# Kernel optimization log

Measured on AMD Instinct MI355X. Metric: run time of the kernel, lower is better.

The kernel has to match this reference:

```python
import jax, jax.numpy as jnp
import numpy as np

BATCH, LEN, DIM = 8, 4096, 512


def setup_inputs() -> dict:
    key = jax.random.key(0)
    k1, k2, k3, k4, k5 = jax.random.split(key, 5)
    x = jax.random.normal(k1, (BATCH, LEN, DIM), dtype=jnp.float32)
    hidden_real = jax.random.normal(k2, (BATCH, DIM), dtype=jnp.float32)
    hidden_imag = jax.random.normal(k3, (BATCH, DIM), dtype=jnp.float32)
    phazor_init = jax.random.normal(k4, (DIM, 2), dtype=jnp.float32)
    phazor_param = jax.random.normal(k5, (DIM, 2), dtype=jnp.float32)
    return {
        "x": x,
        "hidden_real": hidden_real,
        "hidden_imag": hidden_imag,
        "phazor_init": phazor_init,
        "phazor_param": phazor_param,
    }


def _forward(x, hidden, phazor_init, phazor_param):
    L = x.shape[1]
    # view_as_complex of the (dim, 2) real params
    pz = phazor_param[:, 0] + 1j * phazor_param[:, 1]           # [dim] complex
    pi = phazor_init[:, 0] + 1j * phazor_init[:, 1]             # [dim] complex
    # phazor = exp(-|z|^2) * exp(i * angle(z))
    phazor = jnp.exp(-(pz.real * pz.real + pz.imag * pz.imag)) * jnp.exp(1j * jnp.angle(pz))
    # phazor^t for t = 0..L-1  -> [L, dim]
    prog = jnp.power(phazor[None, :], jnp.arange(L, dtype=jnp.float32)[:, None])
    filt = prog * pi[None, :]                                   # [L, dim]
    filt_fft = jnp.fft.fft(filt, n=2 * L, axis=0)               # [2L, dim]
    x_fft = jnp.fft.fft(x.astype(jnp.complex64), n=2 * L, axis=1)  # [B, 2L, dim]
    conv = jnp.fft.ifft(filt_fft[None, :, :] * x_fft, axis=1)[:, :L, :]  # [B, L, dim]
    conv_with_past = conv + hidden[:, None, :] * prog[None, :, :] * phazor[None, None, :]
    return conv_with_past.real, conv_with_past


def reference(x, hidden_real, hidden_imag, phazor_init, phazor_param):
    hidden = hidden_real + 1j * hidden_imag
    out_real, out_complex = _forward(x, hidden, phazor_init, phazor_param)
    return out_real, out_complex
```

## Files before the change

### kernel.cpp

```cpp
#include <hip/hip_runtime.h>
#include <math.h>

#define B 8
#define L 4096
#define D 512
#define LC 64
#define CK (L / LC)
#define BLD ((size_t)B * L * D)

typedef float v2f __attribute__((ext_vector_type(2)));

#define WS_FLOATS (2 * B * CK * D)

__device__ __forceinline__ v2f phazor_of(const float* __restrict__ pparam, int d) {
    float a = pparam[d * 2 + 0];
    float bb = pparam[d * 2 + 1];
    float r2 = fmaf(a, a, bb * bb);
    float inv = rsqrtf(r2);
    inv = inv * fmaf(-0.5f * r2 * inv, inv, 1.5f);
    float mag = __expf(-r2);
    v2f p; p.x = mag * a * inv; p.y = mag * bb * inv;
    return p;
}

__global__ __launch_bounds__(256) void pass1_k(const float* __restrict__ x,
                                               const float* __restrict__ pparam,
                                               float* __restrict__ le) {
    int idx = blockIdx.x * blockDim.x + threadIdx.x;
    int d = idx % D;
    int c = (idx / D) % CK;
    int b = idx / (D * CK);
    v2f ph = phazor_of(pparam, d);
    float ur = 0.f, ui = 0.f;
    const float* xp = x + ((size_t)b * L + (size_t)c * LC) * D + d;
#pragma unroll 8
    for (int i = 0; i < LC; ++i) {
        float xv = xp[(size_t)i * D];
        float nr = fmaf(ph.x, ur, fmaf(-ph.y, ui, xv));
        float ni = fmaf(ph.x, ui, ph.y * ur);
        ur = nr;
        ui = ni;
    }
    v2f lv; lv.x = ur; lv.y = ui;
    *(v2f*)(le + (size_t)idx * 2) = lv;
}

template <int MODE>
__global__ __launch_bounds__(256) void pass2_k(const float* __restrict__ x,
                                               const float* __restrict__ hr,
                                               const float* __restrict__ hi,
                                               const float* __restrict__ pinit,
                                               const float* __restrict__ pparam,
                                               const float* __restrict__ le,
                                               float* __restrict__ out) {
    int idx = blockIdx.x * blockDim.x + threadIdx.x;
    int d = idx % D;
    int c = (idx / D) % CK;
    int b = idx / (D * CK);

    v2f ph = phazor_of(pparam, d);
    v2f q;  q.x = pinit[d * 2 + 0]; q.y = pinit[d * 2 + 1];

    float br = ph.x, bi = ph.y;
#pragma unroll
    for (int s = 0; s < 6; ++s) {
        float sr = fmaf(br, br, -bi * bi);
        float si = 2.f * br * bi;
        br = sr; bi = si;
    }

    float ur = 0.f, ui = 0.f;
    const float* lp = le + (((size_t)b * CK) * D + d) * 2;
    for (int j = 0; j < c; ++j) {
        v2f lv = *(const v2f*)(lp + (size_t)j * D * 2);
        float wr = fmaf(ur, br, fmaf(-ui, bi, lv.x));
        float wi = fmaf(ur, bi, fmaf(ui, br, lv.y));
        ur = wr; ui = wi;
    }

    float pwr = ph.x, pwi = ph.y;
    {
        float er = br, ei = bi;
        int n = c;
#pragma unroll
        for (int s = 0; s < 6; ++s) {
            if (n & 1) {
                float tr = fmaf(pwr, er, -pwi * ei);
                float ti = fmaf(pwr, ei, pwi * er);
                pwr = tr; pwi = ti;
            }
            float sr = fmaf(er, er, -ei * ei);
            float si = 2.f * er * ei;
            er = sr; ei = si;
            n >>= 1;
        }
    }

    float hre = hr[(size_t)b * D + d];
    float him = hi[(size_t)b * D + d];

    const float* xp = x + ((size_t)b * L + (size_t)c * LC) * D + d;
    float* outr = out + ((size_t)b * L + (size_t)c * LC) * D + d;
    float* outr2 = outr + BLD;
    float* outc = out + BLD + (((size_t)b * L + (size_t)c * LC) * D + d) * 2;

#pragma unroll 4
    for (int i = 0; i < LC; ++i) {
        float xv = xp[(size_t)i * D];
        float nr = fmaf(ph.x, ur, fmaf(-ph.y, ui, xv));
        float ni = fmaf(ph.x, ui, ph.y * ur);
        ur = nr;
        ui = ni;
        float vr = fmaf(q.x, ur, fmaf(-q.y, ui, fmaf(hre, pwr, -him * pwi)));
        float vi = fmaf(q.x, ui, fmaf(q.y, ur, fmaf(hre, pwi, him * pwr)));
        outr[(size_t)i * D] = vr;
        if (MODE == 0) {
            outr2[(size_t)i * D] = vr;
        } else {
            v2f vc; vc.x = vr; vc.y = vi;
            *(v2f*)(outc + (size_t)i * D * 2) = vc;
        }
        float tr = fmaf(pwr, ph.x, -pwi * ph.y);
        float ti = fmaf(pwr, ph.y, pwi * ph.x);
        pwr = tr;
        pwi = ti;
    }
}

template <int MODE>
__global__ __launch_bounds__(256) void fallback_k(const float* __restrict__ x,
                                                  const float* __restrict__ hr,
                                                  const float* __restrict__ hi,
                                                  const float* __restrict__ pinit,
                                                  const float* __restrict__ pparam,
                                                  float* __restrict__ out) {
    int idx = blockIdx.x * blockDim.x + threadIdx.x;
    if (idx >= B * D) return;
    int d = idx % D;
    int b = idx / D;
    v2f ph = phazor_of(pparam, d);
    float qr = pinit[d * 2 + 0];
    float qi = pinit[d * 2 + 1];
    float hre = hr[(size_t)b * D + d];
    float him = hi[(size_t)b * D + d];
    float ur = 0.f, ui = 0.f;
    float pwr = ph.x, pwi = ph.y;
    const float* xp = x + (size_t)b * L * D + d;
    float* outr = out + (size_t)b * L * D + d;
    float* outr2 = outr + BLD;
    float* outc = out + BLD + ((size_t)b * L * D + d) * 2;
    for (int t = 0; t < L; ++t) {
        float xv = xp[(size_t)t * D];
        float nr = fmaf(ph.x, ur, fmaf(-ph.y, ui, xv));
        float ni = fmaf(ph.x, ui, ph.y * ur);
        ur = nr; ui = ni;
        float vr = fmaf(qr, ur, fmaf(-qi, ui, fmaf(hre, pwr, -him * pwi)));
        float vi = fmaf(qr, ui, fmaf(qi, ur, fmaf(hre, pwi, him * pwr)));
        outr[(size_t)t * D] = vr;
        if (MODE == 0) {
            outr2[(size_t)t * D] = vr;
        } else {
            v2f vc; vc.x = vr; vc.y = vi;
            *(v2f*)(outc + (size_t)t * D * 2) = vc;
        }
        float tr = fmaf(pwr, ph.x, -pwi * ph.y);
        float ti = fmaf(pwr, ph.y, pwi * ph.x);
        pwr = tr; pwi = ti;
    }
}

extern "C" void kernel_launch(void* const* d_in, const int* in_sizes, int n_in,
                              void* d_out, int out_size, void* d_ws, size_t ws_size,
                              hipStream_t stream) {
    const float* x = (const float*)d_in[0];
    const float* hreal = (const float*)d_in[1];
    const float* himag = (const float*)d_in[2];
    const float* pinit = (const float*)d_in[3];
    const float* pparam = (const float*)d_in[4];
    float* le = (float*)d_ws;
    float* out = (float*)d_out;

    const int mode = (out_size >= (int)(3 * BLD)) ? 1 : 0;
    const bool fast = ws_size >= (size_t)WS_FLOATS * sizeof(float);

    if (fast) {
        int n = B * CK * D;
        pass1_k<<<n / 256, 256, 0, stream>>>(x, pparam, le);
        if (mode == 0)
            pass2_k<0><<<n / 256, 256, 0, stream>>>(x, hreal, himag, pinit, pparam, le, out);
        else
            pass2_k<1><<<n / 256, 256, 0, stream>>>(x, hreal, himag, pinit, pparam, le, out);
    } else {
        int n = B * D;
        if (mode == 0)
            fallback_k<0><<<(n + 255) / 256, 256, 0, stream>>>(x, hreal, himag, pinit, pparam, out);
        else
            fallback_k<1><<<(n + 255) / 256, 256, 0, stream>>>(x, hreal, himag, pinit, pparam, out);
    }
}
```

Baseline: 54.09 us.

## Add sequential carry kernel for chunk prefixes and halve chunk length

Adds a small carry kernel that turns per-chunk local end states into exclusive prefix carries with one sequential pass per (batch, dim). Each pass2 thread then reads its carry directly instead of re-scanning all earlier chunks, which was O(CK) work per thread. Chunk length drops from 64 to 32, doubling parallelism in pass1 and pass2, and the power-by-squaring loop in pass2 grows to 7 steps to cover the larger chunk index. The trade-off is an extra launch and a serial carry kernel of 128 steps with only 4096 threads.

```diff
diff --git a/kernel.cpp b/kernel.cpp
--- a/kernel.cpp
+++ b/kernel.cpp
@@ -4,13 +4,15 @@
 #define B 8
 #define L 4096
 #define D 512
-#define LC 64
+#define LC 32
 #define CK (L / LC)
 #define BLD ((size_t)B * L * D)
 
+#define NTH (B * CK * D)
+
+#define WS_FLOATS (2 * B * CK * D)
+
 typedef float v2f __attribute__((ext_vector_type(2)));
-
-#define WS_FLOATS (2 * B * CK * D)
 
 __device__ __forceinline__ v2f phazor_of(const float* __restrict__ pparam, int d) {
     float a = pparam[d * 2 + 0];
@@ -21,6 +23,18 @@
     float mag = __expf(-r2);
     v2f p; p.x = mag * a * inv; p.y = mag * bb * inv;
     return p;
+}
+
+__device__ __forceinline__ v2f p32_of(v2f ph) {
+    float br = ph.x, bi = ph.y;
+#pragma unroll
+    for (int s = 0; s < 5; ++s) {
+        float sr = fmaf(br, br, -bi * bi);
+        float si = 2.f * br * bi;
+        br = sr; bi = si;
+    }
+    v2f r; r.x = br; r.y = bi;
+    return r;
 }
 
 __global__ __launch_bounds__(256) void pass1_k(const float* __restrict__ x,
@@ -38,11 +52,29 @@
         float xv = xp[(size_t)i * D];
         float nr = fmaf(ph.x, ur, fmaf(-ph.y, ui, xv));
         float ni = fmaf(ph.x, ui, ph.y * ur);
-        ur = nr;
-        ui = ni;
+        ur = nr; ui = ni;
     }
     v2f lv; lv.x = ur; lv.y = ui;
     *(v2f*)(le + (size_t)idx * 2) = lv;
+}
+
+__global__ __launch_bounds__(256) void carry_k(const float* __restrict__ pparam,
+                                               float* __restrict__ le) {
+    int idx = blockIdx.x * blockDim.x + threadIdx.x;
+    int d = idx % D;
+    int b = idx / D;
+    v2f P = p32_of(phazor_of(pparam, d));
+    float wr = 0.f, wi = 0.f;
+    float* lp = le + (((size_t)b * CK) * D + d) * 2;
+#pragma unroll 4
+    for (int c = 0; c < CK; ++c) {
+        v2f lv = *(const v2f*)(lp + (size_t)c * D * 2);
+        v2f wv; wv.x = wr; wv.y = wi;
+        *(v2f*)(lp + (size_t)c * D * 2) = wv;
+        float tr = fmaf(P.x, wr, fmaf(-P.y, wi, lv.x));
+        float ti = fmaf(P.x, wi, fmaf(P.y, wr, lv.y));
+        wr = tr; wi = ti;
+    }
 }
 
 template <int MODE>
@@ -60,30 +92,17 @@
 
     v2f ph = phazor_of(pparam, d);
     v2f q;  q.x = pinit[d * 2 + 0]; q.y = pinit[d * 2 + 1];
-
-    float br = ph.x, bi = ph.y;
-#pragma unroll
-    for (int s = 0; s < 6; ++s) {
-        float sr = fmaf(br, br, -bi * bi);
-        float si = 2.f * br * bi;
-        br = sr; bi = si;
-    }
-
-    float ur = 0.f, ui = 0.f;
-    const float* lp = le + (((size_t)b * CK) * D + d) * 2;
-    for (int j = 0; j < c; ++j) {
-        v2f lv = *(const v2f*)(lp + (size_t)j * D * 2);
-        float wr = fmaf(ur, br, fmaf(-ui, bi, lv.x));
-        float wi = fmaf(ur, bi, fmaf(ui, br, lv.y));
-        ur = wr; ui = wi;
-    }
+    v2f P = p32_of(ph);
+
+    v2f w = *(const v2f*)(le + (size_t)idx * 2);
+    float ur = w.x, ui = w.y;
 
     float pwr = ph.x, pwi = ph.y;
     {
-        float er = br, ei = bi;
+        float er = P.x, ei = P.y;
         int n = c;
 #pragma unroll
-        for (int s = 0; s < 6; ++s) {
+        for (int s = 0; s < 7; ++s) {
             if (n & 1) {
                 float tr = fmaf(pwr, er, -pwi * ei);
                 float ti = fmaf(pwr, ei, pwi * er);
@@ -109,8 +128,7 @@
         float xv = xp[(size_t)i * D];
         float nr = fmaf(ph.x, ur, fmaf(-ph.y, ui, xv));
         float ni = fmaf(ph.x, ui, ph.y * ur);
-        ur = nr;
-        ui = ni;
+        ur = nr; ui = ni;
         float vr = fmaf(q.x, ur, fmaf(-q.y, ui, fmaf(hre, pwr, -him * pwi)));
         float vi = fmaf(q.x, ui, fmaf(q.y, ur, fmaf(hre, pwi, him * pwr)));
         outr[(size_t)i * D] = vr;
@@ -122,8 +140,7 @@
         }
         float tr = fmaf(pwr, ph.x, -pwi * ph.y);
         float ti = fmaf(pwr, ph.y, pwi * ph.x);
-        pwr = tr;
-        pwi = ti;
+        pwr = tr; pwi = ti;
     }
 }
 
@@ -177,19 +194,18 @@
     const float* himag = (const float*)d_in[2];
     const float* pinit = (const float*)d_in[3];
     const float* pparam = (const float*)d_in[4];
-    float* le = (float*)d_ws;
     float* out = (float*)d_out;
 
     const int mode = (out_size >= (int)(3 * BLD)) ? 1 : 0;
-    const bool fast = ws_size >= (size_t)WS_FLOATS * sizeof(float);
-
-    if (fast) {
-        int n = B * CK * D;
-        pass1_k<<<n / 256, 256, 0, stream>>>(x, pparam, le);
+
+    if (ws_size >= (size_t)WS_FLOATS * sizeof(float)) {
+        float* le = (float*)d_ws;
+        pass1_k<<<NTH / 256, 256, 0, stream>>>(x, pparam, le);
+        carry_k<<<(B * D) / 256, 256, 0, stream>>>(pparam, le);
         if (mode == 0)
-            pass2_k<0><<<n / 256, 256, 0, stream>>>(x, hreal, himag, pinit, pparam, le, out);
+            pass2_k<0><<<NTH / 256, 256, 0, stream>>>(x, hreal, himag, pinit, pparam, le, out);
         else
-            pass2_k<1><<<n / 256, 256, 0, stream>>>(x, hreal, himag, pinit, pparam, le, out);
+            pass2_k<1><<<NTH / 256, 256, 0, stream>>>(x, hreal, himag, pinit, pparam, le, out);
     } else {
         int n = B * D;
         if (mode == 0)
```

Result: slower. 62.24 us (+15.1%).
